# Performance work log

Measured on AMD Instinct MI355X. Metric: run time of the kernel, lower is better.

The kernel has to match this reference:

```python
import jax, jax.numpy as jnp
import numpy as np
import math

B, T, C, H, RANK, RD = 8, 512, 2048, 16, 8, 16
HD = C // H  # 128
ADAPTER_SCALE = 1.0 / RANK  # scale / rank with scale=1.0


def setup_inputs() -> dict:
    key = jax.random.key(0)
    ks = jax.random.split(key, 7)
    x = jax.random.normal(ks[0], (B, T, C), dtype=jnp.float32)
    # frozen random linears (weights ~ N(0,1)/sqrt(in_features))
    Wqkv = jax.random.normal(ks[1], (3 * C, C), dtype=jnp.float32) / math.sqrt(C)
    Wout = jax.random.normal(ks[2], (C, C), dtype=jnp.float32) / math.sqrt(C)
    # VeRA frozen random matrices
    A0_qkv = jax.random.normal(ks[3], (RANK, C), dtype=jnp.float32) / math.sqrt(C)
    B0_qkv = jax.random.normal(ks[4], (3 * C, RANK), dtype=jnp.float32) / math.sqrt(RANK)
    A0_out = jax.random.normal(ks[5], (RANK, C), dtype=jnp.float32) / math.sqrt(C)
    B0_out = jax.random.normal(ks[6], (C, RANK), dtype=jnp.float32) / math.sqrt(RANK)
    # learned scaling vectors (init to ones, as in the module)
    d_a_qkv = jnp.ones((RANK,), dtype=jnp.float32)
    d_b_qkv = jnp.ones((RANK,), dtype=jnp.float32)
    d_a_out = jnp.ones((RANK,), dtype=jnp.float32)
    d_b_out = jnp.ones((RANK,), dtype=jnp.float32)
    # partial RoPE caches over first RD dims
    freqs = 1.0 / (10000.0 ** (jnp.arange(0, RD, 2, dtype=jnp.float32) / RD))  # [RD/2]
    ang = jnp.arange(T, dtype=jnp.float32)[:, None] * freqs[None, :]  # [T, RD/2]
    cos = jnp.cos(ang)
    sin = jnp.sin(ang)
    return {"x": x, "Wqkv": Wqkv, "A0_qkv": A0_qkv, "B0_qkv": B0_qkv,
            "d_a_qkv": d_a_qkv, "d_b_qkv": d_b_qkv,
            "Wout": Wout, "A0_out": A0_out, "B0_out": B0_out,
            "d_a_out": d_a_out, "d_b_out": d_b_out,
            "cos": cos, "sin": sin}


def _adapted_linear(x, W, A0, B0, d_a, d_b):
    # frozen(x) + VeRA adapter: diag(d_b) B0 diag(d_a) A0, scaled by 1/rank
    base = x @ W.T
    h = (x @ A0.T) * (d_a * d_b)
    return base + (h @ B0.T) * ADAPTER_SCALE


def _apply_rope(q, cos, sin):
    # q: [B, H, T, HD]; rotate first RD dims, pass-through the rest
    x_rope, x_pass = q[..., :RD], q[..., RD:]
    half = RD // 2
    x1, x2 = x_rope[..., :half], x_rope[..., half:]
    c = cos[None, None]  # [1,1,T,RD/2]
    s = sin[None, None]
    rot = jnp.concatenate([x1 * c - x2 * s, x2 * c + x1 * s], axis=-1)
    return jnp.concatenate([rot, x_pass], axis=-1)


def reference(x, Wqkv, A0_qkv, B0_qkv, d_a_qkv, d_b_qkv,
              Wout, A0_out, B0_out, d_a_out, d_b_out, cos, sin):
    qkv = _adapted_linear(x, Wqkv, A0_qkv, B0_qkv, d_a_qkv, d_b_qkv)  # [B,T,3C]
    qkv = qkv.reshape(B, T, 3, H, HD)
    q = jnp.transpose(qkv[:, :, 0], (0, 2, 1, 3))  # [B,H,T,HD]
    k = jnp.transpose(qkv[:, :, 1], (0, 2, 1, 3))
    v = jnp.transpose(qkv[:, :, 2], (0, 2, 1, 3))
    q = _apply_rope(q, cos, sin)
    k = _apply_rope(k, cos, sin)
    # causal SDPA
    scale = 1.0 / math.sqrt(HD)
    scores = jnp.einsum('bhqd,bhkd->bhqk', q, k) * scale
    mask = jnp.tril(jnp.ones((T, T), dtype=bool))
    scores = jnp.where(mask[None, None], scores, jnp.finfo(scores.dtype).min)
    attn = jax.nn.softmax(scores, axis=-1)
    y = jnp.einsum('bhqk,bhkd->bhqd', attn, v)  # [B,H,T,HD]
    y = jnp.transpose(y, (0, 2, 1, 3)).reshape(B, T, C)
    return _adapted_linear(y, Wout, A0_out, B0_out, d_a_out, d_b_out)
```

## Files before the change

### kernel.cpp

```cpp
#include <hip/hip_runtime.h>

typedef unsigned short ushort_t;
typedef __attribute__((ext_vector_type(8))) short short8;
typedef __attribute__((ext_vector_type(4))) float f32x4;

#define AS1(p) ((const __attribute__((address_space(1))) void*)(p))
#define AS3(p) ((__attribute__((address_space(3))) void*)(p))

__device__ __forceinline__ ushort_t f2bf(float f){
  unsigned u = __float_as_uint(f);
  u += 0x7FFFu + ((u>>16)&1u);
  return (ushort_t)(u>>16);
}
__device__ __forceinline__ float bf2f(ushort_t h){
  return __uint_as_float(((unsigned)h)<<16);
}

__global__ __launch_bounds__(256) void conv_f2b(const float* __restrict__ src,
                                                ushort_t* __restrict__ dst, int n){
  int i = (blockIdx.x*256 + threadIdx.x)*4;
  if (i < n){
    float4 v = *(const float4*)&src[i];
    ushort_t o0=f2bf(v.x), o1=f2bf(v.y), o2=f2bf(v.z), o3=f2bf(v.w);
    ushort4 o; o.x=o0; o.y=o1; o.z=o2; o.w=o3;
    *(ushort4*)&dst[i] = o;
  }
}

__global__ __launch_bounds__(256) void lora_h_f32(const float* __restrict__ X,
                                                  ushort_t* __restrict__ Xbf,
                                                  const float* __restrict__ A0,
                                                  const float* __restrict__ da,
                                                  const float* __restrict__ db,
                                                  float* __restrict__ out, int K){
  int m = blockIdx.x;
  int tid = threadIdx.x, lane = tid & 63, w = tid >> 6;
  float part[8] = {0,0,0,0,0,0,0,0};
  for (int k = tid; k < K; k += 256){
    float xv = X[(size_t)m*K + k];
    Xbf[(size_t)m*K + k] = f2bf(xv);
    #pragma unroll
    for (int r=0;r<8;++r) part[r] += xv * A0[r*K + k];
  }
  #pragma unroll
  for (int r=0;r<8;++r)
    for (int d=1;d<64;d<<=1) part[r] += __shfl_xor(part[r], d, 64);
  __shared__ float wsum[4][8];
  if (lane==0){
    #pragma unroll
    for (int r=0;r<8;++r) wsum[w][r] = part[r];
  }
  __syncthreads();
  if (tid < 8){
    float s = wsum[0][tid]+wsum[1][tid]+wsum[2][tid]+wsum[3][tid];
    out[(size_t)m*8 + tid] = s * da[tid]*db[tid];
  }
}

__global__ __launch_bounds__(256) void lora_h_bf16(const ushort_t* __restrict__ X,
                                                   const float* __restrict__ A0,
                                                   const float* __restrict__ da,
                                                   const float* __restrict__ db,
                                                   float* __restrict__ out, int K){
  int m = blockIdx.x;
  int tid = threadIdx.x, lane = tid & 63, w = tid >> 6;
  float part[8] = {0,0,0,0,0,0,0,0};
  for (int k = tid; k < K; k += 256){
    float xv = bf2f(X[(size_t)m*K + k]);
    #pragma unroll
    for (int r=0;r<8;++r) part[r] += xv * A0[r*K + k];
  }
  #pragma unroll
  for (int r=0;r<8;++r)
    for (int d=1;d<64;d<<=1) part[r] += __shfl_xor(part[r], d, 64);
  __shared__ float wsum[4][8];
  if (lane==0){
    #pragma unroll
    for (int r=0;r<8;++r) wsum[w][r] = part[r];
  }
  __syncthreads();
  if (tid < 8){
    float s = wsum[0][tid]+wsum[1][tid]+wsum[2][tid]+wsum[3][tid];
    out[(size_t)m*8 + tid] = s * da[tid]*db[tid];
  }
}

__global__ __launch_bounds__(512, 1) void gemm256x192_lora(
    const ushort_t* __restrict__ A, const ushort_t* __restrict__ Bw,
    const float* __restrict__ hmat, const float* __restrict__ B0,
    ushort_t* __restrict__ C, int M, int N, int K)
{
  __shared__ __align__(16) char smem[114688];
  const int tid = threadIdx.x, lane = tid & 63, w = tid >> 6;
  const int wm = w >> 1, wn = w & 1;

  const int nbn = N / 192;
  const int nwg = (M >> 8) * nbn;
  const int q8 = nwg >> 3;
  const int swz = ((int)blockIdx.x & 7)*q8 + ((int)blockIdx.x >> 3);
  const int m0 = (swz / nbn) << 8, n0 = (swz % nbn) * 192;

  const int NTt = K >> 6;
  const int srow8  = tid >> 3;
  const int schunk = (lane & 7) ^ (lane >> 3);

  #define STAGE_AU(u, tt, bb) do { \
    const ushort_t* g_ = A + (size_t)(m0 + (u)*64 + srow8)*K + (tt)*64 + schunk*8; \
    __builtin_amdgcn_global_load_lds(AS1(g_), AS3(smem + (bb)*32768 + (u)*8192 + tid*16), 16, 0, 0); \
  } while(0)
  #define STAGE_BU(u, tt, bb) do { \
    const ushort_t* g_ = Bw + (size_t)(n0 + (u)*64 + srow8)*K + (tt)*64 + schunk*8; \
    __builtin_amdgcn_global_load_lds(AS1(g_), AS3(smem + 65536 + (bb)*24576 + (u)*8192 + tid*16), 16, 0, 0); \
  } while(0)

  #define RDA(bb, q, kk) (*(const short8*)(smem + (bb)*32768 + \
      ((q)*64 + wm*16 + (lane&15))*128 + ((((kk)*4 + (lane>>4)) ^ (lane&7))<<4)))
  #define RDB(bb, r, kk) (*(const short8*)(smem + 65536 + (bb)*24576 + \
      ((r)*32 + wn*16 + (lane&15))*128 + ((((kk)*4 + (lane>>4)) ^ (lane&7))<<4)))

  #define MM(q, r, bi) do{ \
    acc[q][r] = __builtin_amdgcn_mfma_f32_16x16x32_bf16(aF[q][0], bF[bi][0], acc[q][r], 0,0,0); \
    acc[q][r] = __builtin_amdgcn_mfma_f32_16x16x32_bf16(aF[q][1], bF[bi][1], acc[q][r], 0,0,0); \
  }while(0)

  #define BARRIER() asm volatile("s_barrier" ::: "memory")

  short8 aF[4][2];
  short8 bF[2][2];
  f32x4 acc[4][6] = {};

  STAGE_AU(0,0,0); STAGE_AU(1,0,0); STAGE_AU(2,0,0); STAGE_AU(3,0,0);
  STAGE_BU(0,0,0); STAGE_BU(1,0,0); STAGE_BU(2,0,0);
  asm volatile("s_waitcnt vmcnt(2)" ::: "memory");
  BARRIER();

  for (int t = 0; t < NTt-1; ++t){
    const int b = t & 1, nb = b ^ 1;
    #pragma unroll
    for (int q=0;q<4;++q){ aF[q][0]=RDA(b,q,0); aF[q][1]=RDA(b,q,1); }
    #pragma unroll
    for (int rl=0;rl<2;++rl){ bF[rl][0]=RDB(b,rl,0); bF[rl][1]=RDB(b,rl,1); }
    STAGE_AU(0,t+1,nb); STAGE_AU(1,t+1,nb);
    __builtin_amdgcn_s_setprio(1);
    MM(0,0,0); MM(0,1,1); MM(1,0,0); MM(1,1,1);
    MM(2,0,0); MM(2,1,1); MM(3,0,0); MM(3,1,1);
    __builtin_amdgcn_s_setprio(0);
    asm volatile("s_waitcnt vmcnt(3)" ::: "memory");
    BARRIER();
    #pragma unroll
    for (int rl=0;rl<2;++rl){ bF[rl][0]=RDB(b,rl+2,0); bF[rl][1]=RDB(b,rl+2,1); }
    STAGE_AU(2,t+1,nb); STAGE_AU(3,t+1,nb); STAGE_BU(0,t+1,nb);
    __builtin_amdgcn_s_setprio(1);
    MM(0,2,0); MM(0,3,1); MM(1,2,0); MM(1,3,1);
    MM(2,2,0); MM(2,3,1); MM(3,2,0); MM(3,3,1);
    __builtin_amdgcn_s_setprio(0);
    asm volatile("s_waitcnt vmcnt(5)" ::: "memory");
    BARRIER();
    #pragma unroll
    for (int rl=0;rl<2;++rl){ bF[rl][0]=RDB(b,rl+4,0); bF[rl][1]=RDB(b,rl+4,1); }
    STAGE_BU(1,t+1,nb); STAGE_BU(2,t+1,nb);
    __builtin_amdgcn_s_setprio(1);
    MM(0,4,0); MM(0,5,1); MM(1,4,0); MM(1,5,1);
    MM(2,4,0); MM(2,5,1); MM(3,4,0); MM(3,5,1);
    __builtin_amdgcn_s_setprio(0);
    asm volatile("s_waitcnt lgkmcnt(0)" ::: "memory");
    asm volatile("s_waitcnt vmcnt(2)" ::: "memory");
    BARRIER();
  }

  {
    const int b = (NTt-1) & 1;
    #pragma unroll
    for (int q=0;q<4;++q){ aF[q][0]=RDA(b,q,0); aF[q][1]=RDA(b,q,1); }
    #pragma unroll
    for (int rl=0;rl<2;++rl){ bF[rl][0]=RDB(b,rl,0); bF[rl][1]=RDB(b,rl,1); }
    __builtin_amdgcn_s_setprio(1);
    MM(0,0,0); MM(0,1,1); MM(1,0,0); MM(1,1,1);
    MM(2,0,0); MM(2,1,1); MM(3,0,0); MM(3,1,1);
    __builtin_amdgcn_s_setprio(0);
    asm volatile("s_waitcnt vmcnt(1)" ::: "memory");
    BARRIER();
    #pragma unroll
    for (int rl=0;rl<2;++rl){ bF[rl][0]=RDB(b,rl+2,0); bF[rl][1]=RDB(b,rl+2,1); }
    __builtin_amdgcn_s_setprio(1);
    MM(0,2,0); MM(0,3,1); MM(1,2,0); MM(1,3,1);
    MM(2,2,0); MM(2,3,1); MM(3,2,0); MM(3,3,1);
    __builtin_amdgcn_s_setprio(0);
    asm volatile("s_waitcnt vmcnt(0)" ::: "memory");
    BARRIER();
    #pragma unroll
    for (int rl=0;rl<2;++rl){ bF[rl][0]=RDB(b,rl+4,0); bF[rl][1]=RDB(b,rl+4,1); }
    MM(0,4,0); MM(0,5,1); MM(1,4,0); MM(1,5,1);
    MM(2,4,0); MM(2,5,1); MM(3,4,0); MM(3,5,1);
  }

  float b0v[6][8];
  #pragma unroll
  for (int r=0;r<6;++r){
    int col = n0 + r*32 + wn*16 + (lane&15);
    const float4* bp = (const float4*)&B0[(size_t)col*8];
    float4 u0 = bp[0], u1 = bp[1];
    b0v[r][0]=u0.x; b0v[r][1]=u0.y; b0v[r][2]=u0.z; b0v[r][3]=u0.w;
    b0v[r][4]=u1.x; b0v[r][5]=u1.y; b0v[r][6]=u1.z; b0v[r][7]=u1.w;
  }
  #pragma unroll
  for (int q=0;q<4;++q){
    #pragma unroll
    for (int jj=0;jj<4;++jj){
      int row = m0 + q*64 + wm*16 + (lane>>4)*4 + jj;
      const float4* hp = (const float4*)&hmat[(size_t)row*8];
      float4 h0 = hp[0], h1 = hp[1];
      #pragma unroll
      for (int r=0;r<6;++r){
        float lor = h0.x*b0v[r][0]+h0.y*b0v[r][1]+h0.z*b0v[r][2]+h0.w*b0v[r][3]
                  + h1.x*b0v[r][4]+h1.y*b0v[r][5]+h1.z*b0v[r][6]+h1.w*b0v[r][7];
        int col = n0 + r*32 + wn*16 + (lane&15);
        C[(size_t)row*N + col] = f2bf(acc[q][r][jj] + 0.125f*lor);
      }
    }
  }
  #undef STAGE_AU
  #undef STAGE_BU
  #undef RDA
  #undef RDB
  #undef MM
  #undef BARRIER
}

template<int MODE>
__global__ __launch_bounds__(512, 1) void gemm128x256_lora(
    const ushort_t* __restrict__ A, const ushort_t* __restrict__ Bw,
    const float* __restrict__ hmat, const float* __restrict__ B0,
    void* __restrict__ C, int M, int N, int K)
{
  __shared__ __align__(16) char smem[98304];
  const int tid = threadIdx.x, lane = tid & 63, w = tid >> 6;
  const int wm = w >> 2, wn = w & 3;

  const int nbn = N >> 8;
  const int nwg = (M >> 7) * nbn;
  const int q8 = nwg >> 3;
  const int swz = ((int)blockIdx.x & 7)*q8 + ((int)blockIdx.x >> 3);
  const int m0 = (swz / nbn) << 7, n0 = (swz % nbn) << 8;

  const int NTt = K >> 6;

  const int srow8  = tid >> 3;
  const int schunk = (lane & 7) ^ (lane >> 3);

  #define STAGE_AU(u, tt, bb) do { \
    const ushort_t* g_ = A + (size_t)(m0 + (u)*64 + srow8)*K + (tt)*64 + schunk*8; \
    __builtin_amdgcn_global_load_lds(AS1(g_), AS3(smem + (bb)*16384 + (u)*8192 + w*1024), 16, 0, 0); \
  } while(0)
  #define STAGE_BU(u, tt, bb) do { \
    const ushort_t* g_ = Bw + (size_t)(n0 + (u)*64 + srow8)*K + (tt)*64 + schunk*8; \
    __builtin_amdgcn_global_load_lds(AS1(g_), AS3(smem + 32768 + (bb)*32768 + (u)*8192 + w*1024), 16, 0, 0); \
  } while(0)

  #define RDA(bb, q, kk) (*(const short8*)(smem + (bb)*16384 + \
      ((q)*32 + wm*16 + (lane&15))*128 + ((((kk)*4 + (lane>>4)) ^ (lane&7))<<4)))
  #define RDB(bb, rg, kk) (*(const short8*)(smem + 32768 + (bb)*32768 + \
      ((rg)*64 + wn*16 + (lane&15))*128 + ((((kk)*4 + (lane>>4)) ^ (lane&7))<<4)))

  #define MM0(q,rl) do{ \
    acc[q][rl] = __builtin_amdgcn_mfma_f32_16x16x32_bf16(aF[q][0], bF[rl][0], acc[q][rl], 0,0,0); \
    acc[q][rl] = __builtin_amdgcn_mfma_f32_16x16x32_bf16(aF[q][1], bF[rl][1], acc[q][rl], 0,0,0); \
  }while(0)
  #define MM1(q,rl) do{ \
    acc[q][(rl)+2] = __builtin_amdgcn_mfma_f32_16x16x32_bf16(aF[q][0], bF[rl][0], acc[q][(rl)+2], 0,0,0); \
    acc[q][(rl)+2] = __builtin_amdgcn_mfma_f32_16x16x32_bf16(aF[q][1], bF[rl][1], acc[q][(rl)+2], 0,0,0); \
  }while(0)

  #define BARRIER() asm volatile("s_barrier" ::: "memory")

  short8 aF[4][2];
  short8 bF[2][2];
  f32x4 acc[4][4] = {};

  STAGE_AU(0,0,0); STAGE_AU(1,0,0); STAGE_BU(0,0,0); STAGE_BU(1,0,0);
  STAGE_BU(2,0,0); STAGE_BU(3,0,0);
  asm volatile("s_waitcnt vmcnt(2)" ::: "memory");
  BARRIER();

  for (int t = 0; t < NTt-1; ++t){
    const int b = t & 1, nb = b ^ 1;
    #pragma unroll
    for (int q=0;q<4;++q){ aF[q][0]=RDA(b,q,0); aF[q][1]=RDA(b,q,1); }
    #pragma unroll
    for (int rl=0;rl<2;++rl){ bF[rl][0]=RDB(b,rl,0); bF[rl][1]=RDB(b,rl,1); }
    STAGE_AU(0,t+1,nb); STAGE_AU(1,t+1,nb); STAGE_BU(0,t+1,nb); STAGE_BU(1,t+1,nb);
    __builtin_amdgcn_s_setprio(1);
    MM0(0,0); MM0(0,1); MM0(1,0); MM0(1,1);
    MM0(2,0); MM0(2,1); MM0(3,0); MM0(3,1);
    __builtin_amdgcn_s_setprio(0);
    asm volatile("s_waitcnt vmcnt(4)" ::: "memory");
    BARRIER();
    #pragma unroll
    for (int rl=0;rl<2;++rl){ bF[rl][0]=RDB(b,rl+2,0); bF[rl][1]=RDB(b,rl+2,1); }
    STAGE_BU(2,t+1,nb); STAGE_BU(3,t+1,nb);
    __builtin_amdgcn_s_setprio(1);
    MM1(0,0); MM1(0,1); MM1(1,0); MM1(1,1);
    MM1(2,0); MM1(2,1); MM1(3,0); MM1(3,1);
    __builtin_amdgcn_s_setprio(0);
    asm volatile("s_waitcnt lgkmcnt(0)" ::: "memory");
    asm volatile("s_waitcnt vmcnt(2)" ::: "memory");
    BARRIER();
  }

  {
    const int b = (NTt-1) & 1;
    #pragma unroll
    for (int q=0;q<4;++q){ aF[q][0]=RDA(b,q,0); aF[q][1]=RDA(b,q,1); }
    #pragma unroll
    for (int rl=0;rl<2;++rl){ bF[rl][0]=RDB(b,rl,0); bF[rl][1]=RDB(b,rl,1); }
    __builtin_amdgcn_s_setprio(1);
    MM0(0,0); MM0(0,1); MM0(1,0); MM0(1,1);
    MM0(2,0); MM0(2,1); MM0(3,0); MM0(3,1);
    __builtin_amdgcn_s_setprio(0);
    asm volatile("s_waitcnt vmcnt(0)" ::: "memory");
    BARRIER();
    #pragma unroll
    for (int rl=0;rl<2;++rl){ bF[rl][0]=RDB(b,rl+2,0); bF[rl][1]=RDB(b,rl+2,1); }
    MM1(0,0); MM1(0,1); MM1(1,0); MM1(1,1);
    MM1(2,0); MM1(2,1); MM1(3,0); MM1(3,1);
  }

  float b0v[4][8];
  #pragma unroll
  for (int r=0;r<4;++r){
    int col = n0 + r*64 + wn*16 + (lane&15);
    const float4* bp = (const float4*)&B0[(size_t)col*8];
    float4 u0 = bp[0], u1 = bp[1];
    b0v[r][0]=u0.x; b0v[r][1]=u0.y; b0v[r][2]=u0.z; b0v[r][3]=u0.w;
    b0v[r][4]=u1.x; b0v[r][5]=u1.y; b0v[r][6]=u1.z; b0v[r][7]=u1.w;
  }
  #pragma unroll
  for (int q=0;q<4;++q){
    #pragma unroll
    for (int jj=0;jj<4;++jj){
      int row = m0 + q*32 + wm*16 + (lane>>4)*4 + jj;
      const float4* hp = (const float4*)&hmat[(size_t)row*8];
      float4 h0 = hp[0], h1 = hp[1];
      #pragma unroll
      for (int r=0;r<4;++r){
        float lor = h0.x*b0v[r][0]+h0.y*b0v[r][1]+h0.z*b0v[r][2]+h0.w*b0v[r][3]
                  + h1.x*b0v[r][4]+h1.y*b0v[r][5]+h1.z*b0v[r][6]+h1.w*b0v[r][7];
        int col = n0 + r*64 + wn*16 + (lane&15);
        float v = acc[q][r][jj] + 0.125f*lor;
        if (MODE==0) ((ushort_t*)C)[(size_t)row*N + col] = f2bf(v);
        else         ((float*)C)[(size_t)row*N + col]    = v;
      }
    }
  }
  #undef STAGE_AU
  #undef STAGE_BU
  #undef RDA
  #undef RDB
  #undef MM0
  #undef MM1
  #undef BARRIER
}

__global__ __launch_bounds__(256) void rope_kernel(ushort_t* __restrict__ qkv,
                                                   const float* __restrict__ cosb,
                                                   const float* __restrict__ sinb){
  int idx = blockIdx.x*256 + threadIdx.x;
  int d = idx & 7;
  int g = idx >> 3;
  int h_ = g & 15;
  int s  = (g>>4) & 1;
  int t  = (g>>5) & 511;
  int b  = g >> 14;
  size_t base = (size_t)(b*512 + t)*6144 + s*2048 + h_*128;
  float x1 = bf2f(qkv[base+d]), x2 = bf2f(qkv[base+d+8]);
  float c = cosb[t*8+d], sn = sinb[t*8+d];
  qkv[base+d]   = f2bf(x1*c - x2*sn);
  qkv[base+d+8] = f2bf(x2*c + x1*sn);
}

__global__ __launch_bounds__(512) void attn_kernel(const ushort_t* __restrict__ qkv,
                                                   ushort_t* __restrict__ y){
  __shared__ __align__(16) ushort_t Ks[2][64*128];
  __shared__ __align__(16) ushort_t Vt[2][128*64];
  __shared__ __align__(16) ushort_t Pl[8][16*64];

  const int flat = blockIdx.x;
  const int qt = ((flat >> 7) ^ ((flat >> 8) & 1)) & 3;
  const int hb = flat & 127;
  const int hh = hb & 15, b = hb >> 4;

  const int tid = threadIdx.x, lane = tid & 63, w = tid >> 6, g = lane >> 4;
  const int qb0 = qt*128;
  const int row_base = b*512;
  const int qoff = hh*128;
  const int koff = 2048 + hh*128;
  const int voff = 4096 + hh*128;
  const float scale = 0.08838834764831845f;

  short8 qf[4];
  {
    int qr = qb0 + w*16 + (lane & 15);
    const ushort_t* qp = qkv + (size_t)(row_base + qr)*6144 + qoff + g*8;
    #pragma unroll
    for (int kc=0;kc<4;++kc) qf[kc] = *(const short8*)(qp + kc*32);
  }

  const int krow = tid >> 4;
  const int kc_  = tid & 15;
  const int kcs  = (kc_ & 8) | ((kc_ ^ (krow & 7)) & 7);
  const int vr   = tid >> 3;
  const int vd0  = (tid & 7) * 16;
  const int vrhi = vr >> 3, vrlo = vr & 7;

  const int nt = 2*qt + 2;
  const int wmin = qb0 + w*16;
  const int wmax = wmin + 15;

  f32x4 o[8] = {};
  float mrow[4] = {-1e30f,-1e30f,-1e30f,-1e30f};
  float lrow[4] = {0,0,0,0};

  short8 vv0, vv1;

  {
    const ushort_t* kg = qkv + (size_t)(row_base + krow)*6144 + koff + kcs*8;
    __builtin_amdgcn_global_load_lds(AS1(kg), AS3((char*)&Ks[0][0] + tid*16), 16, 0, 0);
    __builtin_amdgcn_global_load_lds(AS1(kg + (size_t)32*6144), AS3((char*)&Ks[0][0] + 8192 + tid*16), 16, 0, 0);
    const ushort_t* vg = qkv + (size_t)(row_base + vr)*6144 + voff + vd0;
    vv0 = ((const short8*)vg)[0];
    vv1 = ((const short8*)vg)[1];
    #pragma unroll
    for (int ii=0;ii<8;++ii){
      int sw = (vrhi ^ ii) << 3;
      Vt[0][(vd0 + ii    )*64 + sw + vrlo] = (ushort_t)vv0[ii];
      Vt[0][(vd0 + 8 + ii)*64 + sw + vrlo] = (ushort_t)vv1[ii];
    }
  }
  __syncthreads();

  for (int t = 0; t < nt; ++t){
    const int bb = t & 1, nb = bb ^ 1;
    const int kv0 = t*64;
    const bool have_next = (t+1 < nt);

    if (have_next){
      const int kv1 = kv0 + 64;
      const ushort_t* kg = qkv + (size_t)(row_base + kv1 + krow)*6144 + koff + kcs*8;
      __builtin_amdgcn_global_load_lds(AS1(kg), AS3((char*)&Ks[nb][0] + tid*16), 16, 0, 0);
      __builtin_amdgcn_global_load_lds(AS1(kg + (size_t)32*6144), AS3((char*)&Ks[nb][0] + 8192 + tid*16), 16, 0, 0);
      const ushort_t* vg = qkv + (size_t)(row_base + kv1 + vr)*6144 + voff + vd0;
      vv0 = ((const short8*)vg)[0];
      vv1 = ((const short8*)vg)[1];
    }

    if (kv0 <= wmax){
      f32x4 s4[4] = {};
      #pragma unroll
      for (int cg=0;cg<4;++cg){
        const int row = cg*16 + (lane&15);
        const int rx = row & 7;
        #pragma unroll
        for (int kc=0;kc<4;++kc){
          const int ch = kc*4 + g;
          const short8 kfv = *(const short8*)&Ks[bb][row*128 + (((ch&8)|((ch^rx)&7))<<3)];
          s4[cg] = __builtin_amdgcn_mfma_f32_16x16x32_bf16(qf[kc], kfv, s4[cg], 0, 0, 0);
        }
      }

      const bool diag = (kv0 + 63 > wmin);
      float aa[4][4];
      float mx4[4];
      int needR = 0;
      #pragma unroll
      for (int j=0;j<4;++j){
        float a0 = s4[0][j]*scale, a1 = s4[1][j]*scale, a2 = s4[2][j]*scale, a3 = s4[3][j]*scale;
        if (diag){
          int q_abs = wmin + g*4 + j;
          int c0 = kv0 + (lane&15);
          if (c0      > q_abs) a0 = -1e30f;
          if (c0 + 16 > q_abs) a1 = -1e30f;
          if (c0 + 32 > q_abs) a2 = -1e30f;
          if (c0 + 48 > q_abs) a3 = -1e30f;
        }
        aa[j][0]=a0; aa[j][1]=a1; aa[j][2]=a2; aa[j][3]=a3;
        float mx = fmaxf(fmaxf(a0,a1), fmaxf(a2,a3));
        #pragma unroll
        for (int d=1; d<16; d<<=1) mx = fmaxf(mx, __shfl_xor(mx, d, 16));
        mx4[j] = mx;
        needR |= (mx > mrow[j] + 8.0f) ? 1 : 0;
      }
      needR = __any(needR);

      float p0[4], p1[4], p2[4], p3[4];
      if (needR){
        #pragma unroll
        for (int j=0;j<4;++j){
          float mn = fmaxf(mrow[j], mx4[j]);
          float f  = __expf(mrow[j] - mn);
          mrow[j] = mn;
          p0[j] = __expf(aa[j][0] - mn); p1[j] = __expf(aa[j][1] - mn);
          p2[j] = __expf(aa[j][2] - mn); p3[j] = __expf(aa[j][3] - mn);
          float rs = p0[j] + p1[j] + p2[j] + p3[j];
          #pragma unroll
          for (int d=1; d<16; d<<=1) rs += __shfl_xor(rs, d, 16);
          lrow[j] = lrow[j]*f + rs;
          #pragma unroll
          for (int n=0;n<8;++n) o[n][j] *= f;
        }
      } else {
        #pragma unroll
        for (int j=0;j<4;++j){
          p0[j] = __expf(aa[j][0] - mrow[j]); p1[j] = __expf(aa[j][1] - mrow[j]);
          p2[j] = __expf(aa[j][2] - mrow[j]); p3[j] = __expf(aa[j][3] - mrow[j]);
          float rs = p0[j] + p1[j] + p2[j] + p3[j];
          #pragma unroll
          for (int d=1; d<16; d<<=1) rs += __shfl_xor(rs, d, 16);
          lrow[j] += rs;
        }
      }

      {
        ushort_t* plw = &Pl[w][0];
        #pragma unroll
        for (int j=0;j<4;++j){
          const int prow = g*4 + j;
          const int rx = prow & 7;
          const int cl = (lane&15)>>3, c7 = lane&7;
          plw[prow*64 + (((0*2+cl)^rx)<<3) + c7] = f2bf(p0[j]);
          plw[prow*64 + (((1*2+cl)^rx)<<3) + c7] = f2bf(p1[j]);
          plw[prow*64 + (((2*2+cl)^rx)<<3) + c7] = f2bf(p2[j]);
          plw[prow*64 + (((3*2+cl)^rx)<<3) + c7] = f2bf(p3[j]);
        }
      }
      {
        const ushort_t* plw = &Pl[w][0];
        const int rowP = lane & 15, rxp = rowP & 7;
        const short8 pf0 = *(const short8*)&plw[rowP*64 + (((g  )^rxp)<<3)];
        const short8 pf1 = *(const short8*)&plw[rowP*64 + (((4+g)^rxp)<<3)];
        #pragma unroll
        for (int n=0;n<8;++n){
          const int d = n*16 + (lane&15);
          const int dx = d & 7;
          const short8 vf0 = *(const short8*)&Vt[bb][d*64 + (((g  )^dx)<<3)];
          const short8 vf1 = *(const short8*)&Vt[bb][d*64 + (((4+g)^dx)<<3)];
          o[n] = __builtin_amdgcn_mfma_f32_16x16x32_bf16(pf0, vf0, o[n], 0, 0, 0);
          o[n] = __builtin_amdgcn_mfma_f32_16x16x32_bf16(pf1, vf1, o[n], 0, 0, 0);
        }
      }
    }

    if (have_next){
      #pragma unroll
      for (int ii=0;ii<8;++ii){
        int sw = (vrhi ^ ii) << 3;
        Vt[nb][(vd0 + ii    )*64 + sw + vrlo] = (ushort_t)vv0[ii];
        Vt[nb][(vd0 + 8 + ii)*64 + sw + vrlo] = (ushort_t)vv1[ii];
      }
    }
    __syncthreads();
  }

  #pragma unroll
  for (int j=0;j<4;++j){
    float inv = 1.0f / lrow[j];
    int qr = qb0 + w*16 + g*4 + j;
    #pragma unroll
    for (int n=0;n<8;++n)
      y[(size_t)(row_base+qr)*2048 + hh*128 + n*16 + (lane&15)] = f2bf(o[n][j]*inv);
  }
}

extern "C" void kernel_launch(void* const* d_in, const int* in_sizes, int n_in,
                              void* d_out, int out_size, void* d_ws, size_t ws_size,
                              hipStream_t stream){
  const float* x       = (const float*)d_in[0];
  const float* Wqkv    = (const float*)d_in[1];
  const float* A0_qkv  = (const float*)d_in[2];
  const float* B0_qkv  = (const float*)d_in[3];
  const float* da_qkv  = (const float*)d_in[4];
  const float* db_qkv  = (const float*)d_in[5];
  const float* Wout    = (const float*)d_in[6];
  const float* A0_out  = (const float*)d_in[7];
  const float* B0_out  = (const float*)d_in[8];
  const float* da_out  = (const float*)d_in[9];
  const float* db_out  = (const float*)d_in[10];
  const float* cosb    = (const float*)d_in[11];
  const float* sinb    = (const float*)d_in[12];
  float* out = (float*)d_out;

  char* ws = (char*)d_ws;
  ushort_t* x_bf    = (ushort_t*)(ws);
  ushort_t* wqkv_bf = (ushort_t*)(ws + 16777216);
  ushort_t* wout_bf = (ushort_t*)(ws + 41943040);
  ushort_t* qkv_bf  = (ushort_t*)(ws + 50331648);
  ushort_t* y_bf    = (ushort_t*)(ws + 100663296);
  float*    h_qkv   = (float*)   (ws + 117440512);
  float*    h_out   = (float*)   (ws + 117571584);

  const int M = 4096;
  const int C = 2048;
  const int N3 = 6144;

  conv_f2b<<<12288,256, 0, stream>>>(Wqkv, wqkv_bf, N3*C);
  conv_f2b<<<4096, 256, 0, stream>>>(Wout, wout_bf, C*C);

  lora_h_f32<<<M, 256, 0, stream>>>(x, x_bf, A0_qkv, da_qkv, db_qkv, h_qkv, C);

  gemm256x192_lora<<<(M/256)*(N3/192), 512, 0, stream>>>(x_bf, wqkv_bf, h_qkv, B0_qkv,
                                                         qkv_bf, M, N3, C);

  rope_kernel<<<4096, 256, 0, stream>>>(qkv_bf, cosb, sinb);

  attn_kernel<<<512, 512, 0, stream>>>(qkv_bf, y_bf);

  lora_h_bf16<<<M, 256, 0, stream>>>(y_bf, A0_out, da_out, db_out, h_out, C);

  gemm128x256_lora<1><<<(M/128)*(C/256), 512, 0, stream>>>(y_bf, wout_bf, h_out, B0_out,
                                                           out, M, C, C);
}
```

Measured before the change: 227.3 us.

## Fuse output LoRA down-projection into attention epilogue with per-head partial reduction

The attention kernel now computes per-head partial products of its normalized fp32 output with A0_out and writes them to a scratch buffer. A small reduction kernel sums the 16 head partials and applies the d_a*d_b scaling. This replaces the separate lora_h_bf16 pass, which reread the whole bf16 attention output. The cost is extra shuffles and A0 loads in the attention epilogue, plus a tiny extra launch.

```diff
diff --git a/kernel.cpp b/kernel.cpp
--- a/kernel.cpp
+++ b/kernel.cpp
@@ -57,32 +57,16 @@
   }
 }
 
-__global__ __launch_bounds__(256) void lora_h_bf16(const ushort_t* __restrict__ X,
-                                                   const float* __restrict__ A0,
+__global__ __launch_bounds__(256) void lora_reduce(const float* __restrict__ hpart,
                                                    const float* __restrict__ da,
                                                    const float* __restrict__ db,
-                                                   float* __restrict__ out, int K){
-  int m = blockIdx.x;
-  int tid = threadIdx.x, lane = tid & 63, w = tid >> 6;
-  float part[8] = {0,0,0,0,0,0,0,0};
-  for (int k = tid; k < K; k += 256){
-    float xv = bf2f(X[(size_t)m*K + k]);
-    #pragma unroll
-    for (int r=0;r<8;++r) part[r] += xv * A0[r*K + k];
-  }
-  #pragma unroll
-  for (int r=0;r<8;++r)
-    for (int d=1;d<64;d<<=1) part[r] += __shfl_xor(part[r], d, 64);
-  __shared__ float wsum[4][8];
-  if (lane==0){
-    #pragma unroll
-    for (int r=0;r<8;++r) wsum[w][r] = part[r];
-  }
-  __syncthreads();
-  if (tid < 8){
-    float s = wsum[0][tid]+wsum[1][tid]+wsum[2][tid]+wsum[3][tid];
-    out[(size_t)m*8 + tid] = s * da[tid]*db[tid];
-  }
+                                                   float* __restrict__ out){
+  int i = blockIdx.x*256 + threadIdx.x;
+  int r = i & 7;
+  float s = 0.f;
+  #pragma unroll
+  for (int hh=0; hh<16; ++hh) s += hpart[(size_t)hh*32768 + i];
+  out[i] = s * da[r]*db[r];
 }
 
 __global__ __launch_bounds__(512, 1) void gemm256x192_lora(
@@ -379,7 +363,9 @@
 }
 
 __global__ __launch_bounds__(512) void attn_kernel(const ushort_t* __restrict__ qkv,
-                                                   ushort_t* __restrict__ y){
+                                                   ushort_t* __restrict__ y,
+                                                   const float* __restrict__ A0o,
+                                                   float* __restrict__ hpart){
   __shared__ __align__(16) ushort_t Ks[2][64*128];
   __shared__ __align__(16) ushort_t Vt[2][128*64];
   __shared__ __align__(16) ushort_t Pl[8][16*64];
@@ -560,13 +546,37 @@
     __syncthreads();
   }
 
+  float invj[4];
+  #pragma unroll
+  for (int j=0;j<4;++j) invj[j] = 1.0f / lrow[j];
+
   #pragma unroll
   for (int j=0;j<4;++j){
-    float inv = 1.0f / lrow[j];
     int qr = qb0 + w*16 + g*4 + j;
     #pragma unroll
     for (int n=0;n<8;++n)
-      y[(size_t)(row_base+qr)*2048 + hh*128 + n*16 + (lane&15)] = f2bf(o[n][j]*inv);
+      y[(size_t)(row_base+qr)*2048 + hh*128 + n*16 + (lane&15)] = f2bf(o[n][j]*invj[j]);
+  }
+
+  #pragma unroll
+  for (int r=0;r<8;++r){
+    float a0v[8];
+    #pragma unroll
+    for (int n=0;n<8;++n)
+      a0v[n] = A0o[(size_t)r*2048 + hh*128 + n*16 + (lane&15)];
+    #pragma unroll
+    for (int j=0;j<4;++j){
+      float s = 0.f;
+      #pragma unroll
+      for (int n=0;n<8;++n) s += o[n][j]*a0v[n];
+      s *= invj[j];
+      #pragma unroll
+      for (int d=1; d<16; d<<=1) s += __shfl_xor(s, d, 16);
+      if ((lane & 15) == 0){
+        int qr = qb0 + w*16 + g*4 + j;
+        hpart[((size_t)hh*4096 + row_base + qr)*8 + r] = s;
+      }
+    }
   }
 }
 
@@ -596,6 +606,7 @@
   ushort_t* y_bf    = (ushort_t*)(ws + 100663296);
   float*    h_qkv   = (float*)   (ws + 117440512);
   float*    h_out   = (float*)   (ws + 117571584);
+  float*    h_part  = (float*)   (ws + 117702656);
 
   const int M = 4096;
   const int C = 2048;
@@ -611,9 +622,9 @@
 
   rope_kernel<<<4096, 256, 0, stream>>>(qkv_bf, cosb, sinb);
 
-  attn_kernel<<<512, 512, 0, stream>>>(qkv_bf, y_bf);
-
-  lora_h_bf16<<<M, 256, 0, stream>>>(y_bf, A0_out, da_out, db_out, h_out, C);
+  attn_kernel<<<512, 512, 0, stream>>>(qkv_bf, y_bf, A0_out, h_part);
+
+  lora_reduce<<<128, 256, 0, stream>>>(h_part, da_out, db_out, h_out);
 
   gemm128x256_lora<1><<<(M/128)*(C/256), 512, 0, stream>>>(y_bf, wout_bf, h_out, B0_out,
                                                            out, M, C, C);
```

Result: no change. 227.1 us, median of 2 (-0.1%).
